# Kernel tuning notes

Measured on AMD Instinct MI355X. Metric: run time of the kernel, lower is better.

Reference implementation:

```python
import jax, jax.numpy as jnp
import numpy as np

MIXTURE_COUNT = 4
GAUSSIANS_PER_MIXTURE = 4
EM_ITERS = 3
EPS = 1e-4


def setup_inputs() -> dict:
    key = jax.random.key(0)
    k1, k2 = jax.random.split(key)
    B, C, N = 1, 3, 1048576
    input_tensor = jax.random.normal(k1, (B, C, N), dtype=jnp.float32)
    label_tensor = jax.random.randint(k2, (B, N), 0, MIXTURE_COUNT, dtype=jnp.int32)
    return {"input_tensor": input_tensor, "label_tensor": label_tensor}


def _gmm_em(x, mix_oh, M, G):
    # x: [B,N,C] features, mix_oh: [B,N,M] one-hot mixture labels
    B, N, C = x.shape
    eye = jnp.eye(C, dtype=x.dtype)
    # init: split each mixture's pixels round-robin across its G gaussians
    sub_oh = jax.nn.one_hot(jnp.arange(N) % G, G, dtype=x.dtype)  # [N,G]
    resp = mix_oh[:, :, :, None] * sub_oh[None, :, None, :]       # [B,N,M,G]
    logp = None
    for _ in range(EM_ITERS):
        # ---- M-step: label-segmented weighted stats ----
        w = resp.sum(axis=1) + EPS                                 # [B,M,G]
        mu = jnp.einsum('bnmg,bnc->bmgc', resp, x) / w[..., None]  # [B,M,G,C]
        xx = jnp.einsum('bnmg,bnc,bnd->bmgcd', resp, x, x) / w[..., None, None]
        cov = xx - mu[..., :, None] * mu[..., None, :] + EPS * eye  # [B,M,G,C,C]
        prec = jnp.linalg.inv(cov)
        _, logdet = jnp.linalg.slogdet(cov)                        # [B,M,G]
        pi = w / w.sum(axis=2, keepdims=True)                      # [B,M,G]
        # ---- E-step: per-pixel Gaussian log-likelihoods ----
        # Mahalanobis via expansion to avoid [B,N,M,G,C] residual tensor
        xPx = jnp.einsum('bnc,bmgcd,bnd->bnmg', x, prec, x)
        xPm = jnp.einsum('bnc,bmgcd,bmgd->bnmg', x, prec, mu)
        mPm = jnp.einsum('bmgc,bmgcd,bmgd->bmg', mu, prec, mu)
        quad = xPx - 2.0 * xPm + mPm[:, None]                      # [B,N,M,G]
        logp = (jnp.log(pi)[:, None]
                - 0.5 * (quad + logdet[:, None] + C * jnp.log(2.0 * jnp.pi)))
        # pixels only redistribute among the gaussians of their own mixture
        resp = mix_oh[..., None] * jax.nn.softmax(logp, axis=3)
    return logp


def reference(input_tensor, label_tensor):
    M, G = MIXTURE_COUNT, GAUSSIANS_PER_MIXTURE
    x = jnp.swapaxes(input_tensor, 1, 2)                           # [B,N,C]
    mix_oh = jax.nn.one_hot(label_tensor, M, dtype=x.dtype)        # [B,N,M]
    logp = _gmm_em(x, mix_oh, M, G)                                # [B,N,M,G]
    # posterior over mixtures for every pixel
    mix_log = jax.nn.logsumexp(logp, axis=3)                       # [B,N,M]
    post = jax.nn.softmax(mix_log, axis=2)
    return jnp.swapaxes(post, 1, 2)                                # [B,M,N]
```

## Files before the change

kernel.cpp:

```cpp
#include <hip/hip_runtime.h>
#include <math.h>


#define NTHR  256
#define NBLK  512
#define EPS_F 1e-4f
#define LOG2PI3 5.5136311992280366f


static __device__ void compute_params(const float* __restrict__ sumsIn,
                                      float* spar, float* sums, float* wtab,
                                      int tid) {
    if (tid < 160) {
        float4 v = ((const float4*)sumsIn)[tid];
        sums[tid] = (v.x + v.y) + (v.z + v.w);
    }
    __syncthreads();
    if (tid < 16) wtab[tid] = sums[tid * 10] + EPS_F;
    __syncthreads();
    if (tid < 16) {
        const int tt = tid;
        const float* S = &sums[tt * 10];
        const float w  = wtab[tt];
        const float iw = 1.0f / w;
        float mu0 = S[1] * iw, mu1 = S[2] * iw, mu2 = S[3] * iw;
        float c00 = S[4] * iw - mu0 * mu0 + EPS_F;
        float c01 = S[5] * iw - mu0 * mu1;
        float c02 = S[6] * iw - mu0 * mu2;
        float c11 = S[7] * iw - mu1 * mu1 + EPS_F;
        float c12 = S[8] * iw - mu1 * mu2;
        float c22 = S[9] * iw - mu2 * mu2 + EPS_F;
        float d00 = c11 * c22 - c12 * c12;
        float d01 = c02 * c12 - c01 * c22;
        float d02 = c01 * c12 - c02 * c11;
        float det = c00 * d00 + c01 * d01 + c02 * d02;
        float idet = 1.0f / det;
        float P00 = d00 * idet, P01 = d01 * idet, P02 = d02 * idet;
        float P11 = (c00 * c22 - c02 * c02) * idet;
        float P12 = (c01 * c02 - c00 * c12) * idet;
        float P22 = (c00 * c11 - c01 * c01) * idet;
        float logdet = logf(det);
        const int mb = tt & 12;
        float wsum = wtab[mb] + wtab[mb + 1] + wtab[mb + 2] + wtab[mb + 3];
        float logpi = logf(w) - logf(wsum);
        float pm0 = P00 * mu0 + P01 * mu1 + P02 * mu2;
        float pm1 = P01 * mu0 + P11 * mu1 + P12 * mu2;
        float pm2 = P02 * mu0 + P12 * mu1 + P22 * mu2;
        float mPm = mu0 * pm0 + mu1 * pm1 + mu2 * pm2;
        float c0 = logpi - 0.5f * (mPm + logdet + LOG2PI3);
        float* P = spar + tt * 12;
        P[0] = pm0; P[1] = pm1; P[2] = pm2; P[3] = c0;
        P[4] = -0.5f * P00; P[5] = -0.5f * P11; P[6] = -0.5f * P22;
        P[7] = -P01; P[8] = -P02; P[9] = -P12;
        P[10] = 0.f; P[11] = 0.f;
    }
    __syncthreads();
}

__global__ __launch_bounds__(NTHR, 2) void k_accum(const float* __restrict__ x,
                                                   const int* __restrict__ lab,
                                                   const float* __restrict__ sumsIn,
                                                   float* __restrict__ sumsOut,
                                                   int N, int mode) {
    __shared__ __align__(16) float spar[192];
    __shared__ float sums[160];
    __shared__ float wtab[16];
    __shared__ float sred[NTHR / 64][160];
    const int tid  = threadIdx.x;
    const int wave = tid >> 6, lane = tid & 63;
    const int q    = lane & 3;
    const int qb   = lane & ~3;
    if (mode) compute_params(sumsIn, spar, sums, wtab, tid);

    float acc[40];
    #pragma unroll
    for (int k = 0; k < 40; ++k) acc[k] = 0.f;

    const int groups = N >> 2;
    const int stride = gridDim.x * NTHR;
    const int gid    = blockIdx.x * NTHR + tid;
    const int trips  = (groups + stride - 1) / stride;
    const float4* x0p = (const float4*)x;
    const float4* x1p = (const float4*)(x + N);
    const float4* x2p = (const float4*)(x + 2 * N);
    const int4*   lp  = (const int4*)lab;

    for (int tr = 0; tr < trips; ++tr) {
        const int i  = tr * stride + gid;
        const bool valid = i < groups;
        const int ii = valid ? i : 0;
        float4 va = x0p[ii], vb = x1p[ii], vc = x2p[ii];
        int4   m4 = lp[ii];
        float pa[4] = {va.x, va.y, va.z, va.w};
        float pb[4] = {vb.x, vb.y, vb.z, vb.w};
        float pc[4] = {vc.x, vc.y, vc.z, vc.w};
        int   pm[4] = {m4.x, m4.y, m4.z, m4.w};
        if (!valid) { pm[0] = pm[1] = pm[2] = pm[3] = -1; }

        #pragma unroll
        for (int j = 0; j < 4; ++j) {
            const float a = pa[j], b = pb[j], c = pc[j];
            const int   m = pm[j];
            float ws[4] = {0.f, 0.f, 0.f, 0.f};
            if (mode) {
                const float* P0 = spar + (m & 3) * 48;
                float l[4];
                #pragma unroll
                for (int g = 0; g < 4; ++g) {
                    const float* P = P0 + g * 12;
                    float4 q0 = *(const float4*)(P);
                    float4 q1 = *(const float4*)(P + 4);
                    float2 q2 = *(const float2*)(P + 8);
                    l[g] = q0.w + q0.x * a + q0.y * b + q0.z * c
                         + q1.x * (a * a) + q1.y * (b * b) + q1.z * (c * c)
                         + q1.w * (a * b) + q2.x * (a * c) + q2.y * (b * c);
                }
                float mx = fmaxf(fmaxf(l[0], l[1]), fmaxf(l[2], l[3]));
                float e0 = __expf(l[0] - mx), e1 = __expf(l[1] - mx);
                float e2 = __expf(l[2] - mx), e3 = __expf(l[3] - mx);
                float rs = 1.0f / (e0 + e1 + e2 + e3);
                ws[0] = e0 * rs; ws[1] = e1 * rs; ws[2] = e2 * rs; ws[3] = e3 * rs;
            }
            #pragma unroll
            for (int src = 0; src < 4; ++src) {
                const float ra = __shfl(a, qb + src, 64);
                const float rb = __shfl(b, qb + src, 64);
                const float rc = __shfl(c, qb + src, 64);
                const int   rm = __shfl(m, qb + src, 64);
                const bool sel = (rm == q);
                const float aa = ra * ra, ab = ra * rb, ac = ra * rc;
                const float bb = rb * rb, bc = rb * rc, cc = rc * rc;
                if (mode) {
                    float rw[4];
                    rw[0] = __shfl(ws[0], qb + src, 64);
                    rw[1] = __shfl(ws[1], qb + src, 64);
                    rw[2] = __shfl(ws[2], qb + src, 64);
                    rw[3] = __shfl(ws[3], qb + src, 64);
                    #pragma unroll
                    for (int g = 0; g < 4; ++g) {
                        const float s = sel ? rw[g] : 0.f;
                        float* A = &acc[g * 10];
                        A[0] += s;
                        A[1] = fmaf(s, ra, A[1]);
                        A[2] = fmaf(s, rb, A[2]);
                        A[3] = fmaf(s, rc, A[3]);
                        A[4] = fmaf(s, aa, A[4]);
                        A[5] = fmaf(s, ab, A[5]);
                        A[6] = fmaf(s, ac, A[6]);
                        A[7] = fmaf(s, bb, A[7]);
                        A[8] = fmaf(s, bc, A[8]);
                        A[9] = fmaf(s, cc, A[9]);
                    }
                } else {
                    const float s = sel ? 1.f : 0.f;
                    float* A = &acc[j * 10];
                    A[0] += s;
                    A[1] = fmaf(s, ra, A[1]);
                    A[2] = fmaf(s, rb, A[2]);
                    A[3] = fmaf(s, rc, A[3]);
                    A[4] = fmaf(s, aa, A[4]);
                    A[5] = fmaf(s, ab, A[5]);
                    A[6] = fmaf(s, ac, A[6]);
                    A[7] = fmaf(s, bb, A[7]);
                    A[8] = fmaf(s, bc, A[8]);
                    A[9] = fmaf(s, cc, A[9]);
                }
            }
        }
    }

    #pragma unroll
    for (int k = 0; k < 40; ++k) {
        float v = acc[k];
        v += __shfl_xor(v,  4, 64);
        v += __shfl_xor(v,  8, 64);
        v += __shfl_xor(v, 16, 64);
        v += __shfl_xor(v, 32, 64);
        acc[k] = v;
    }
    if (lane < 4) {
        #pragma unroll
        for (int k = 0; k < 40; ++k) sred[wave][lane * 40 + k] = acc[k];
    }
    __syncthreads();
    if (tid < 160) {
        float s = sred[0][tid] + sred[1][tid] + sred[2][tid] + sred[3][tid];
        unsafeAtomicAdd(&sumsOut[tid * 4 + (blockIdx.x & 3)], s);
    }
}

__global__ __launch_bounds__(NTHR, 2) void k_final(const float* __restrict__ x,
                                                   const float* __restrict__ sumsIn,
                                                   float* __restrict__ out,
                                                   int N) {
    __shared__ __align__(16) float spar[192];
    __shared__ float sums[160];
    __shared__ float wtab[16];
    compute_params(sumsIn, spar, sums, wtab, threadIdx.x);
    const int lane = threadIdx.x & 63;
    const int q    = lane & 3;
    const int qb   = lane & ~3;
    float PR[40];
    #pragma unroll
    for (int g = 0; g < 4; ++g)
        #pragma unroll
        for (int k = 0; k < 10; ++k) PR[g * 10 + k] = spar[q * 48 + g * 12 + k];

    const int groups = N >> 2;
    const int stride = gridDim.x * NTHR;
    const int gid    = blockIdx.x * NTHR + threadIdx.x;
    const int trips  = (groups + stride - 1) / stride;
    const float4* x0p = (const float4*)x;
    const float4* x1p = (const float4*)(x + N);
    const float4* x2p = (const float4*)(x + 2 * N);

    for (int tr = 0; tr < trips; ++tr) {
        const int i  = tr * stride + gid;
        const bool valid = i < groups;
        const int ii = valid ? i : 0;
        float4 va = x0p[ii], vb = x1p[ii], vc = x2p[ii];
        float pa[4] = {va.x, va.y, va.z, va.w};
        float pb[4] = {vb.x, vb.y, vb.z, vb.w};
        float pc[4] = {vc.x, vc.y, vc.z, vc.w};
        float po[4][4];

        #pragma unroll
        for (int j = 0; j < 4; ++j) {
            const float a = pa[j], b = pb[j], c = pc[j];
            float M[4];
            #pragma unroll
            for (int p = 0; p < 4; ++p) {
                const float ra = __shfl(a, qb + p, 64);
                const float rb = __shfl(b, qb + p, 64);
                const float rc = __shfl(c, qb + p, 64);
                const float aa = ra * ra, ab = ra * rb, ac = ra * rc;
                const float bb = rb * rb, bc = rb * rc, cc = rc * rc;
                float l[4];
                #pragma unroll
                for (int g = 0; g < 4; ++g) {
                    const float* P = &PR[g * 10];
                    l[g] = P[3] + P[0] * ra + P[1] * rb + P[2] * rc
                         + P[4] * aa + P[5] * bb + P[6] * cc
                         + P[7] * ab + P[8] * ac + P[9] * bc;
                }
                float mx = fmaxf(fmaxf(l[0], l[1]), fmaxf(l[2], l[3]));
                M[p] = mx + __logf(__expf(l[0] - mx) + __expf(l[1] - mx)
                                 + __expf(l[2] - mx) + __expf(l[3] - mx));
            }
            float W[4] = {0.f, 0.f, 0.f, 0.f};
            #pragma unroll
            for (int k = 0; k < 4; ++k) {
                #pragma unroll
                for (int qq = 0; qq < 4; ++qq) {
                    float v = __shfl(M[k], qb + qq, 64);
                    if (q == k) W[qq] = v;
                }
            }
            float mmx = fmaxf(fmaxf(W[0], W[1]), fmaxf(W[2], W[3]));
            float e0 = __expf(W[0] - mmx), e1 = __expf(W[1] - mmx);
            float e2 = __expf(W[2] - mmx), e3 = __expf(W[3] - mmx);
            float rs = 1.0f / (e0 + e1 + e2 + e3);
            po[j][0] = e0 * rs; po[j][1] = e1 * rs;
            po[j][2] = e2 * rs; po[j][3] = e3 * rs;
        }
        if (valid) {
            #pragma unroll
            for (int m = 0; m < 4; ++m) {
                ((float4*)(out + (size_t)m * N))[i] =
                    make_float4(po[0][m], po[1][m], po[2][m], po[3][m]);
            }
        }
    }
}

extern "C" void kernel_launch(void* const* d_in, const int* in_sizes, int n_in,
                              void* d_out, int out_size, void* d_ws, size_t ws_size,
                              hipStream_t stream) {
    const float* x   = (const float*)d_in[0];
    const int*   lab = (const int*)d_in[1];
    float* out = (float*)d_out;
    const int N = in_sizes[1];

    float* sums = (float*)d_ws;
    hipMemsetAsync(sums, 0, 3 * 640 * sizeof(float), stream);

    dim3 grid(NBLK), blk(NTHR);
    k_accum<<<grid, blk, 0, stream>>>(x, lab, sums, sums, N, 0);
    k_accum<<<grid, blk, 0, stream>>>(x, lab, sums, sums + 640, N, 1);
    k_accum<<<grid, blk, 0, stream>>>(x, lab, sums + 640, sums + 1280, N, 1);
    k_final<<<grid, blk, 0, stream>>>(x, sums + 1280, out, N);
}
```

Baseline: 151.7 us.

## Compute responsibilities only for owning lane, use DPP quad broadcasts, split init kernel

Result: slower. 184.3 us (+21.5%).

```diff
diff --git a/kernel.cpp b/kernel.cpp
--- a/kernel.cpp
+++ b/kernel.cpp
@@ -3,9 +3,19 @@
 
 
 #define NTHR  256
-#define NBLK  512
+#define NBLK  1024
 #define EPS_F 1e-4f
 #define LOG2PI3 5.5136311992280366f
+
+template <int S>
+static __device__ __forceinline__ float qbcast(float v) {
+    return __int_as_float(__builtin_amdgcn_update_dpp(
+        0, __float_as_int(v), (S * 0x55), 0xF, 0xF, true));
+}
+template <int S>
+static __device__ __forceinline__ int qbcast_i(int v) {
+    return __builtin_amdgcn_update_dpp(0, v, (S * 0x55), 0xF, 0xF, true);
+}
 
 
 static __device__ void compute_params(const float* __restrict__ sumsIn,
@@ -57,11 +67,91 @@
     __syncthreads();
 }
 
+static __device__ __forceinline__ void reduce_out(float* acc, float (*sred)[160],
+                                                  float* __restrict__ sumsOut,
+                                                  int tid, int wave, int lane) {
+    #pragma unroll
+    for (int k = 0; k < 40; ++k) {
+        float v = acc[k];
+        v += __shfl_xor(v,  4, 64);
+        v += __shfl_xor(v,  8, 64);
+        v += __shfl_xor(v, 16, 64);
+        v += __shfl_xor(v, 32, 64);
+        acc[k] = v;
+    }
+    if (lane < 4) {
+        #pragma unroll
+        for (int k = 0; k < 40; ++k) sred[wave][lane * 40 + k] = acc[k];
+    }
+    __syncthreads();
+    if (tid < 160) {
+        float s = sred[0][tid] + sred[1][tid] + sred[2][tid] + sred[3][tid];
+        unsafeAtomicAdd(&sumsOut[tid * 4 + 0], s);
+    }
+}
+
+__global__ __launch_bounds__(NTHR, 2) void k_accum0(const float* __restrict__ x,
+                                                    const int* __restrict__ lab,
+                                                    float* __restrict__ sumsOut,
+                                                    int N) {
+    __shared__ float sred[NTHR / 64][160];
+    const int tid  = threadIdx.x;
+    const int wave = tid >> 6, lane = tid & 63;
+    const int q    = lane & 3;
+
+    float acc[40];
+    #pragma unroll
+    for (int k = 0; k < 40; ++k) acc[k] = 0.f;
+
+    const int groups = N >> 2;
+    const int stride = gridDim.x * NTHR;
+    const int gid    = blockIdx.x * NTHR + tid;
+    const float4* x0p = (const float4*)x;
+    const float4* x1p = (const float4*)(x + N);
+    const float4* x2p = (const float4*)(x + 2 * N);
+    const int4*   lp  = (const int4*)lab;
+
+    for (int i = gid; i < groups; i += stride) {
+        float4 va = x0p[i], vb = x1p[i], vc = x2p[i];
+        int4   m4 = lp[i];
+        float pa[4] = {va.x, va.y, va.z, va.w};
+        float pb[4] = {vb.x, vb.y, vb.z, vb.w};
+        float pc[4] = {vc.x, vc.y, vc.z, vc.w};
+        int   pm[4] = {m4.x, m4.y, m4.z, m4.w};
+        #pragma unroll
+        for (int j = 0; j < 4; ++j) {
+            const float a = pa[j], b = pb[j], c = pc[j];
+            const int   m = pm[j];
+            float ra[4], rb[4], rc[4]; int rm[4];
+            ra[0]=qbcast<0>(a); rb[0]=qbcast<0>(b); rc[0]=qbcast<0>(c); rm[0]=qbcast_i<0>(m);
+            ra[1]=qbcast<1>(a); rb[1]=qbcast<1>(b); rc[1]=qbcast<1>(c); rm[1]=qbcast_i<1>(m);
+            ra[2]=qbcast<2>(a); rb[2]=qbcast<2>(b); rc[2]=qbcast<2>(c); rm[2]=qbcast_i<2>(m);
+            ra[3]=qbcast<3>(a); rb[3]=qbcast<3>(b); rc[3]=qbcast<3>(c); rm[3]=qbcast_i<3>(m);
+            #pragma unroll
+            for (int p = 0; p < 4; ++p) {
+                if (rm[p] == q) {
+                    const float A = ra[p], B = rb[p], C = rc[p];
+                    float* Q = &acc[j * 10];
+                    Q[0] += 1.f;
+                    Q[1] += A;  Q[2] += B;  Q[3] += C;
+                    Q[4] = fmaf(A, A, Q[4]);
+                    Q[5] = fmaf(A, B, Q[5]);
+                    Q[6] = fmaf(A, C, Q[6]);
+                    Q[7] = fmaf(B, B, Q[7]);
+                    Q[8] = fmaf(B, C, Q[8]);
+                    Q[9] = fmaf(C, C, Q[9]);
+                }
+            }
+        }
+    }
+    reduce_out(acc, sred, sumsOut, tid, wave, lane);
+}
+
 __global__ __launch_bounds__(NTHR, 2) void k_accum(const float* __restrict__ x,
                                                    const int* __restrict__ lab,
                                                    const float* __restrict__ sumsIn,
                                                    float* __restrict__ sumsOut,
-                                                   int N, int mode) {
+                                                   int N) {
     __shared__ __align__(16) float spar[192];
     __shared__ float sums[160];
     __shared__ float wtab[16];
@@ -69,8 +159,13 @@
     const int tid  = threadIdx.x;
     const int wave = tid >> 6, lane = tid & 63;
     const int q    = lane & 3;
-    const int qb   = lane & ~3;
-    if (mode) compute_params(sumsIn, spar, sums, wtab, tid);
+    compute_params(sumsIn, spar, sums, wtab, tid);
+
+    float PR[40];
+    #pragma unroll
+    for (int g = 0; g < 4; ++g)
+        #pragma unroll
+        for (int k = 0; k < 10; ++k) PR[g * 10 + k] = spar[q * 48 + g * 12 + k];
 
     float acc[40];
     #pragma unroll
@@ -79,114 +174,66 @@
     const int groups = N >> 2;
     const int stride = gridDim.x * NTHR;
     const int gid    = blockIdx.x * NTHR + tid;
-    const int trips  = (groups + stride - 1) / stride;
     const float4* x0p = (const float4*)x;
     const float4* x1p = (const float4*)(x + N);
     const float4* x2p = (const float4*)(x + 2 * N);
     const int4*   lp  = (const int4*)lab;
 
-    for (int tr = 0; tr < trips; ++tr) {
-        const int i  = tr * stride + gid;
-        const bool valid = i < groups;
-        const int ii = valid ? i : 0;
-        float4 va = x0p[ii], vb = x1p[ii], vc = x2p[ii];
-        int4   m4 = lp[ii];
+    for (int i = gid; i < groups; i += stride) {
+        float4 va = x0p[i], vb = x1p[i], vc = x2p[i];
+        int4   m4 = lp[i];
         float pa[4] = {va.x, va.y, va.z, va.w};
         float pb[4] = {vb.x, vb.y, vb.z, vb.w};
         float pc[4] = {vc.x, vc.y, vc.z, vc.w};
         int   pm[4] = {m4.x, m4.y, m4.z, m4.w};
-        if (!valid) { pm[0] = pm[1] = pm[2] = pm[3] = -1; }
-
         #pragma unroll
         for (int j = 0; j < 4; ++j) {
             const float a = pa[j], b = pb[j], c = pc[j];
             const int   m = pm[j];
-            float ws[4] = {0.f, 0.f, 0.f, 0.f};
-            if (mode) {
-                const float* P0 = spar + (m & 3) * 48;
-                float l[4];
-                #pragma unroll
-                for (int g = 0; g < 4; ++g) {
-                    const float* P = P0 + g * 12;
-                    float4 q0 = *(const float4*)(P);
-                    float4 q1 = *(const float4*)(P + 4);
-                    float2 q2 = *(const float2*)(P + 8);
-                    l[g] = q0.w + q0.x * a + q0.y * b + q0.z * c
-                         + q1.x * (a * a) + q1.y * (b * b) + q1.z * (c * c)
-                         + q1.w * (a * b) + q2.x * (a * c) + q2.y * (b * c);
-                }
-                float mx = fmaxf(fmaxf(l[0], l[1]), fmaxf(l[2], l[3]));
-                float e0 = __expf(l[0] - mx), e1 = __expf(l[1] - mx);
-                float e2 = __expf(l[2] - mx), e3 = __expf(l[3] - mx);
-                float rs = 1.0f / (e0 + e1 + e2 + e3);
-                ws[0] = e0 * rs; ws[1] = e1 * rs; ws[2] = e2 * rs; ws[3] = e3 * rs;
-            }
+            float ra[4], rb[4], rc[4]; int rm[4];
+            ra[0]=qbcast<0>(a); rb[0]=qbcast<0>(b); rc[0]=qbcast<0>(c); rm[0]=qbcast_i<0>(m);
+            ra[1]=qbcast<1>(a); rb[1]=qbcast<1>(b); rc[1]=qbcast<1>(c); rm[1]=qbcast_i<1>(m);
+            ra[2]=qbcast<2>(a); rb[2]=qbcast<2>(b); rc[2]=qbcast<2>(c); rm[2]=qbcast_i<2>(m);
+            ra[3]=qbcast<3>(a); rb[3]=qbcast<3>(b); rc[3]=qbcast<3>(c); rm[3]=qbcast_i<3>(m);
             #pragma unroll
-            for (int src = 0; src < 4; ++src) {
-                const float ra = __shfl(a, qb + src, 64);
-                const float rb = __shfl(b, qb + src, 64);
-                const float rc = __shfl(c, qb + src, 64);
-                const int   rm = __shfl(m, qb + src, 64);
-                const bool sel = (rm == q);
-                const float aa = ra * ra, ab = ra * rb, ac = ra * rc;
-                const float bb = rb * rb, bc = rb * rc, cc = rc * rc;
-                if (mode) {
-                    float rw[4];
-                    rw[0] = __shfl(ws[0], qb + src, 64);
-                    rw[1] = __shfl(ws[1], qb + src, 64);
-                    rw[2] = __shfl(ws[2], qb + src, 64);
-                    rw[3] = __shfl(ws[3], qb + src, 64);
+            for (int p = 0; p < 4; ++p) {
+                if (rm[p] == q) {
+                    const float A = ra[p], B = rb[p], C = rc[p];
+                    const float aa = A * A, ab = A * B, ac = A * C;
+                    const float bb = B * B, bc = B * C, cc = C * C;
+                    float l[4];
                     #pragma unroll
                     for (int g = 0; g < 4; ++g) {
-                        const float s = sel ? rw[g] : 0.f;
-                        float* A = &acc[g * 10];
-                        A[0] += s;
-                        A[1] = fmaf(s, ra, A[1]);
-                        A[2] = fmaf(s, rb, A[2]);
-                        A[3] = fmaf(s, rc, A[3]);
-                        A[4] = fmaf(s, aa, A[4]);
-                        A[5] = fmaf(s, ab, A[5]);
-                        A[6] = fmaf(s, ac, A[6]);
-                        A[7] = fmaf(s, bb, A[7]);
-                        A[8] = fmaf(s, bc, A[8]);
-                        A[9] = fmaf(s, cc, A[9]);
+                        const float* P = &PR[g * 10];
+                        l[g] = P[3] + P[0] * A + P[1] * B + P[2] * C
+                             + P[4] * aa + P[5] * bb + P[6] * cc
+                             + P[7] * ab + P[8] * ac + P[9] * bc;
                     }
-                } else {
-                    const float s = sel ? 1.f : 0.f;
-                    float* A = &acc[j * 10];
-                    A[0] += s;
-                    A[1] = fmaf(s, ra, A[1]);
-                    A[2] = fmaf(s, rb, A[2]);
-                    A[3] = fmaf(s, rc, A[3]);
-                    A[4] = fmaf(s, aa, A[4]);
-                    A[5] = fmaf(s, ab, A[5]);
-                    A[6] = fmaf(s, ac, A[6]);
-                    A[7] = fmaf(s, bb, A[7]);
-                    A[8] = fmaf(s, bc, A[8]);
-                    A[9] = fmaf(s, cc, A[9]);
+                    float mx = fmaxf(fmaxf(l[0], l[1]), fmaxf(l[2], l[3]));
+                    float e0 = __expf(l[0] - mx), e1 = __expf(l[1] - mx);
+                    float e2 = __expf(l[2] - mx), e3 = __expf(l[3] - mx);
+                    float rs = 1.0f / (e0 + e1 + e2 + e3);
+                    float w[4] = {e0 * rs, e1 * rs, e2 * rs, e3 * rs};
+                    #pragma unroll
+                    for (int g = 0; g < 4; ++g) {
+                        const float s = w[g];
+                        float* Q = &acc[g * 10];
+                        Q[0] += s;
+                        Q[1] = fmaf(s, A,  Q[1]);
+                        Q[2] = fmaf(s, B,  Q[2]);
+                        Q[3] = fmaf(s, C,  Q[3]);
+                        Q[4] = fmaf(s, aa, Q[4]);
+                        Q[5] = fmaf(s, ab, Q[5]);
+                        Q[6] = fmaf(s, ac, Q[6]);
+                        Q[7] = fmaf(s, bb, Q[7]);
+                        Q[8] = fmaf(s, bc, Q[8]);
+                        Q[9] = fmaf(s, cc, Q[9]);
+                    }
                 }
             }
         }
     }
-
-    #pragma unroll
-    for (int k = 0; k < 40; ++k) {
-        float v = acc[k];
-        v += __shfl_xor(v,  4, 64);
-        v += __shfl_xor(v,  8, 64);
-        v += __shfl_xor(v, 16, 64);
-        v += __shfl_xor(v, 32, 64);
-        acc[k] = v;
-    }
-    if (lane < 4) {
-        #pragma unroll
-        for (int k = 0; k < 40; ++k) sred[wave][lane * 40 + k] = acc[k];
-    }
-    __syncthreads();
-    if (tid < 160) {
-        float s = sred[0][tid] + sred[1][tid] + sred[2][tid] + sred[3][tid];
-        unsafeAtomicAdd(&sumsOut[tid * 4 + (blockIdx.x & 3)], s);
-    }
+    reduce_out(acc, sred, sumsOut, tid, wave, lane);
 }
 
 __global__ __launch_bounds__(NTHR, 2) void k_final(const float* __restrict__ x,
@@ -199,7 +246,6 @@
     compute_params(sumsIn, spar, sums, wtab, threadIdx.x);
     const int lane = threadIdx.x & 63;
     const int q    = lane & 3;
-    const int qb   = lane & ~3;
     float PR[40];
     #pragma unroll
     for (int g = 0; g < 4; ++g)
@@ -209,37 +255,34 @@
     const int groups = N >> 2;
     const int stride = gridDim.x * NTHR;
     const int gid    = blockIdx.x * NTHR + threadIdx.x;
-    const int trips  = (groups + stride - 1) / stride;
     const float4* x0p = (const float4*)x;
     const float4* x1p = (const float4*)(x + N);
     const float4* x2p = (const float4*)(x + 2 * N);
 
-    for (int tr = 0; tr < trips; ++tr) {
-        const int i  = tr * stride + gid;
-        const bool valid = i < groups;
-        const int ii = valid ? i : 0;
-        float4 va = x0p[ii], vb = x1p[ii], vc = x2p[ii];
+    for (int i = gid; i < groups; i += stride) {
+        float4 va = x0p[i], vb = x1p[i], vc = x2p[i];
         float pa[4] = {va.x, va.y, va.z, va.w};
         float pb[4] = {vb.x, vb.y, vb.z, vb.w};
         float pc[4] = {vc.x, vc.y, vc.z, vc.w};
         float po[4][4];
-
         #pragma unroll
         for (int j = 0; j < 4; ++j) {
             const float a = pa[j], b = pb[j], c = pc[j];
             float M[4];
             #pragma unroll
             for (int p = 0; p < 4; ++p) {
-                const float ra = __shfl(a, qb + p, 64);
-                const float rb = __shfl(b, qb + p, 64);
-                const float rc = __shfl(c, qb + p, 64);
-                const float aa = ra * ra, ab = ra * rb, ac = ra * rc;
-                const float bb = rb * rb, bc = rb * rc, cc = rc * rc;
+                float A, B, C;
+                if (p == 0) { A=qbcast<0>(a); B=qbcast<0>(b); C=qbcast<0>(c); }
+                if (p == 1) { A=qbcast<1>(a); B=qbcast<1>(b); C=qbcast<1>(c); }
+                if (p == 2) { A=qbcast<2>(a); B=qbcast<2>(b); C=qbcast<2>(c); }
+                if (p == 3) { A=qbcast<3>(a); B=qbcast<3>(b); C=qbcast<3>(c); }
+                const float aa = A * A, ab = A * B, ac = A * C;
+                const float bb = B * B, bc = B * C, cc = C * C;
                 float l[4];
                 #pragma unroll
                 for (int g = 0; g < 4; ++g) {
                     const float* P = &PR[g * 10];
-                    l[g] = P[3] + P[0] * ra + P[1] * rb + P[2] * rc
+                    l[g] = P[3] + P[0] * A + P[1] * B + P[2] * C
                          + P[4] * aa + P[5] * bb + P[6] * cc
                          + P[7] * ab + P[8] * ac + P[9] * bc;
                 }
@@ -247,14 +290,15 @@
                 M[p] = mx + __logf(__expf(l[0] - mx) + __expf(l[1] - mx)
                                  + __expf(l[2] - mx) + __expf(l[3] - mx));
             }
-            float W[4] = {0.f, 0.f, 0.f, 0.f};
+            float W[4];
             #pragma unroll
-            for (int k = 0; k < 4; ++k) {
-                #pragma unroll
-                for (int qq = 0; qq < 4; ++qq) {
-                    float v = __shfl(M[k], qb + qq, 64);
-                    if (q == k) W[qq] = v;
-                }
+            for (int qq = 0; qq < 4; ++qq) {
+                float v0, v1, v2, v3;
+                if (qq == 0) { v0=qbcast<0>(M[0]); v1=qbcast<0>(M[1]); v2=qbcast<0>(M[2]); v3=qbcast<0>(M[3]); }
+                if (qq == 1) { v0=qbcast<1>(M[0]); v1=qbcast<1>(M[1]); v2=qbcast<1>(M[2]); v3=qbcast<1>(M[3]); }
+                if (qq == 2) { v0=qbcast<2>(M[0]); v1=qbcast<2>(M[1]); v2=qbcast<2>(M[2]); v3=qbcast<2>(M[3]); }
+                if (qq == 3) { v0=qbcast<3>(M[0]); v1=qbcast<3>(M[1]); v2=qbcast<3>(M[2]); v3=qbcast<3>(M[3]); }
+                W[qq] = (q == 0) ? v0 : ((q == 1) ? v1 : ((q == 2) ? v2 : v3));
             }
             float mmx = fmaxf(fmaxf(W[0], W[1]), fmaxf(W[2], W[3]));
             float e0 = __expf(W[0] - mmx), e1 = __expf(W[1] - mmx);
@@ -263,12 +307,10 @@
             po[j][0] = e0 * rs; po[j][1] = e1 * rs;
             po[j][2] = e2 * rs; po[j][3] = e3 * rs;
         }
-        if (valid) {
-            #pragma unroll
-            for (int m = 0; m < 4; ++m) {
-                ((float4*)(out + (size_t)m * N))[i] =
-                    make_float4(po[0][m], po[1][m], po[2][m], po[3][m]);
-            }
+        #pragma unroll
+        for (int m = 0; m < 4; ++m) {
+            ((float4*)(out + (size_t)m * N))[i] =
+                make_float4(po[0][m], po[1][m], po[2][m], po[3][m]);
         }
     }
 }
@@ -285,8 +327,8 @@
     hipMemsetAsync(sums, 0, 3 * 640 * sizeof(float), stream);
 
     dim3 grid(NBLK), blk(NTHR);
-    k_accum<<<grid, blk, 0, stream>>>(x, lab, sums, sums, N, 0);
-    k_accum<<<grid, blk, 0, stream>>>(x, lab, sums, sums + 640, N, 1);
-    k_accum<<<grid, blk, 0, stream>>>(x, lab, sums + 640, sums + 1280, N, 1);
-    k_final<<<grid, blk, 0, stream>>>(x, sums + 1280, out, N);
-}
+    k_accum0<<<grid, blk, 0, stream>>>(x, lab, sums, N);
+    k_accum <<<grid, blk, 0, stream>>>(x, lab, sums, sums + 640, N);
+    k_accum <<<grid, blk, 0, stream>>>(x, lab, sums + 640, sums + 1280, N);
+    k_final <<<grid, blk, 0, stream>>>(x, sums + 1280, out, N);
+}
```
